# Kernel optimization log

Hardware: AMD Instinct MI355X
Metric: run time of the kernel (lower is better)

Reference implementation:

```python
import math
import jax, jax.numpy as jnp
import numpy as np

B, S, D = 64, 729, 64  # S = (32*14//16 - 1)**2

def setup_inputs() -> dict:
    key = jax.random.key(0)
    kq, kk, kv, km = jax.random.split(key, 4)
    return {
        "query": jax.random.normal(kq, (B, S, D), dtype=jnp.float32),
        "key": jax.random.normal(kk, (B, S, D), dtype=jnp.float32),
        "value": jax.random.normal(kv, (B, S, D), dtype=jnp.float32),
        "mask": jax.random.randint(km, (B, S, S), 0, 2, dtype=jnp.int32),
    }

def reference(query, key, value, mask):
    dk = query.shape[-1]
    # [B,S,S] scores
    scores = jnp.einsum('bqd,bkd->bqk', query, key) / math.sqrt(dk)
    scores = jnp.where(mask == 0, jnp.float32(-1e9), scores)
    attention = jnp.tanh(scores)  # args.activation == 'tanh'
    # ignore_diag == 1: zero the diagonal of each [S,S] attention map
    eye = jnp.eye(attention.shape[-1], dtype=attention.dtype)
    attention = attention * (1.0 - eye)
    out = jnp.einsum('bqk,bkd->bqd', attention, value)
    return (out, attention)
```

## Files before the change

### kernel.cpp

```cpp
#include <hip/hip_runtime.h>

#define BATCH 64
#define SEQ 729
#define DIM 64
#define NT 12
#define STRB 72
#define STRW 68

typedef __attribute__((ext_vector_type(8))) short bf16x8;
typedef __attribute__((ext_vector_type(4))) float f32x4;
typedef int   i32x4a __attribute__((ext_vector_type(4), aligned(4)));
typedef float f32x4a __attribute__((ext_vector_type(4), aligned(4)));

__device__ __forceinline__ unsigned short f2bf(float f) {
    unsigned int u = __float_as_uint(f);
    u += 0x7fffu + ((u >> 16) & 1u);
    return (unsigned short)(u >> 16);
}

__device__ __forceinline__ unsigned long long pack4bf(float a, float b, float c, float d) {
    return (unsigned long long)f2bf(a)
         | ((unsigned long long)f2bf(b) << 16)
         | ((unsigned long long)f2bf(c) << 32)
         | ((unsigned long long)f2bf(d) << 48);
}

__device__ __forceinline__ float fast_tanh(float x) {
    float e = __builtin_amdgcn_exp2f(x * 2.88539008177792681f);
    return 1.0f - 2.0f * __builtin_amdgcn_rcpf(e + 1.0f);
}

#define BAR() do { \
    asm volatile("s_waitcnt lgkmcnt(0)" ::: "memory"); \
    __builtin_amdgcn_s_barrier(); \
    __builtin_amdgcn_sched_barrier(0); \
} while (0)

__global__ __launch_bounds__(256, 3) void attn_kernel(
    const float* __restrict__ Qg, const float* __restrict__ Kg,
    const float* __restrict__ Vg, const int* __restrict__ Mg,
    float* __restrict__ Og, float* __restrict__ Ag)
{
    __shared__ unsigned short Ks[64 * STRB];
    __shared__ unsigned short Vs[64 * STRB];
    __shared__ unsigned short Qs[64 * STRB];
    __shared__ float Pf[64 * STRW];
    int* Mint = (int*)Pf;

    const int tid = threadIdx.x;
    const int q0  = blockIdx.x * 64;
    const int b   = blockIdx.y;

    const float* Qb = Qg + (size_t)b * SEQ * DIM;
    const float* Kb = Kg + (size_t)b * SEQ * DIM;
    const float* Vb = Vg + (size_t)b * SEQ * DIM;
    const int*   Mb = Mg + (size_t)b * SEQ * SEQ;
    float* Ob = Og + (size_t)b * SEQ * DIM;
    float* Ab = Ag + (size_t)b * SEQ * SEQ;

    const int lane = tid & 63;
    const int quad = lane >> 4;
    const int l15  = lane & 15;
    const int qrow = (tid >> 6) * 16;

    const int rr = tid >> 4;
    const int cc = (tid & 15) * 4;
    const int vd0 = (tid & 15) * 4;
    const int vk0 = (tid >> 4) * 4;
    const int prow = qrow + (lane >> 4);
    const int pcol = (lane & 15) * 4;

    float4 kr[4], vr[4];
    i32x4a mr[4];

    auto load_k = [&](int k0n) {
        #pragma unroll
        for (int i = 0; i < 4; ++i) {
            int gk = k0n + rr + 16 * i;
            kr[i] = (gk < SEQ) ? *(const float4*)(Kb + gk * DIM + cc)
                               : float4{0, 0, 0, 0};
        }
    };
    auto load_v = [&](int k0n) {
        #pragma unroll
        for (int i = 0; i < 4; ++i) {
            int gk = k0n + vk0 + i;
            vr[i] = (gk < SEQ) ? *(const float4*)(Vb + gk * DIM + vd0)
                               : float4{0, 0, 0, 0};
        }
    };
    auto load_mask = [&](int k0n) {
        #pragma unroll
        for (int i = 0; i < 4; ++i) {
            int gq = q0 + prow + 4 * i;
            int gk = k0n + pcol;
            if (gq < SEQ && gk + 3 < SEQ) {
                mr[i] = *(const i32x4a*)(Mb + (size_t)gq * SEQ + gk);
            } else if (gq < SEQ) {
                i32x4a t;
                #pragma unroll
                for (int e = 0; e < 4; ++e)
                    t[e] = (gk + e < SEQ) ? Mb[(size_t)gq * SEQ + gk + e] : 0;
                mr[i] = t;
            } else {
                mr[i] = i32x4a{0, 0, 0, 0};
            }
        }
    };
    auto drain_mask = [&]() {
        #pragma unroll
        for (int i = 0; i < 4; ++i)
            *(i32x4a*)&Mint[(prow + 4 * i) * STRW + pcol] = mr[i];
    };
    auto drain_kv = [&]() {
        #pragma unroll
        for (int i = 0; i < 4; ++i)
            *(unsigned long long*)&Ks[(rr + 16 * i) * STRB + cc] =
                pack4bf(kr[i].x, kr[i].y, kr[i].z, kr[i].w);
        #pragma unroll
        for (int j = 0; j < 4; ++j) {
            float v0 = j==0?vr[0].x:j==1?vr[0].y:j==2?vr[0].z:vr[0].w;
            float v1 = j==0?vr[1].x:j==1?vr[1].y:j==2?vr[1].z:vr[1].w;
            float v2 = j==0?vr[2].x:j==1?vr[2].y:j==2?vr[2].z:vr[2].w;
            float v3 = j==0?vr[3].x:j==1?vr[3].y:j==2?vr[3].z:vr[3].w;
            *(unsigned long long*)&Vs[(vd0 + j) * STRB + vk0] = pack4bf(v0, v1, v2, v3);
        }
    };

    #pragma unroll
    for (int i = 0; i < 4; ++i) {
        int gq = q0 + rr + 16 * i;
        float4 x = (gq < SEQ) ? *(const float4*)(Qb + gq * DIM + cc)
                              : float4{0, 0, 0, 0};
        *(unsigned long long*)&Qs[(rr + 16 * i) * STRB + cc] = pack4bf(x.x, x.y, x.z, x.w);
    }
    BAR();

    const bf16x8 aq0 = *(const bf16x8*)&Qs[(qrow + l15) * STRB + quad * 8];
    const bf16x8 aq1 = *(const bf16x8*)&Qs[(qrow + l15) * STRB + 32 + quad * 8];

    load_k(0); load_v(0); load_mask(0);

    f32x4 oacc[4];
    #pragma unroll
    for (int dt = 0; dt < 4; ++dt) {
        oacc[dt][0]=0.f; oacc[dt][1]=0.f; oacc[dt][2]=0.f; oacc[dt][3]=0.f;
    }

    for (int kt = 0; kt < NT; ++kt) {
        const int k0 = kt * 64;

        BAR();
        drain_mask();
        drain_kv();
        BAR();

        if (kt + 1 < NT) {
            load_k(k0 + 64); load_v(k0 + 64); load_mask(k0 + 64);
        }

        f32x4 sacc[4];
        #pragma unroll
        for (int nt2 = 0; nt2 < 4; ++nt2) {
            bf16x8 bk0 = *(const bf16x8*)&Ks[(nt2 * 16 + l15) * STRB + quad * 8];
            bf16x8 bk1 = *(const bf16x8*)&Ks[(nt2 * 16 + l15) * STRB + 32 + quad * 8];
            f32x4 c; c[0]=0.f; c[1]=0.f; c[2]=0.f; c[3]=0.f;
            c = __builtin_amdgcn_mfma_f32_16x16x32_bf16(aq0, bk0, c, 0, 0, 0);
            c = __builtin_amdgcn_mfma_f32_16x16x32_bf16(aq1, bk1, c, 0, 0, 0);
            sacc[nt2] = c;
        }

        #pragma unroll
        for (int nt2 = 0; nt2 < 4; ++nt2) {
            int col = nt2 * 16 + l15;
            int gk  = k0 + col;
            #pragma unroll
            for (int r = 0; r < 4; ++r) {
                int qloc = qrow + quad * 4 + r;
                int gq = q0 + qloc;
                int m = Mint[qloc * STRW + col];
                float sv = sacc[nt2][r] * 0.125f;
                bool msk = (m == 0);
                float p = fast_tanh(msk ? -1e9f : sv);
                if (msk) p = -1.0f;
                if (gq == gk) p = 0.0f;
                if (gq >= SEQ || gk >= SEQ) p = 0.0f;
                Pf[qloc * STRW + col] = p;
                Qs[qloc * STRB + col] = f2bf(p);
            }
        }

        #pragma unroll
        for (int i = 0; i < 4; ++i) {
            int row = prow + 4 * i;
            int gq  = q0 + row;
            int gk  = k0 + pcol;
            f32x4 pv = *(const f32x4*)&Pf[row * STRW + pcol];
            if (gq < SEQ) {
                if (gk + 3 < SEQ) {
                    *(f32x4a*)(Ab + (size_t)gq * SEQ + gk) = pv;
                } else {
                    #pragma unroll
                    for (int e = 0; e < 4; ++e)
                        if (gk + e < SEQ) Ab[(size_t)gq * SEQ + gk + e] = pv[e];
                }
            }
        }

        const bf16x8 ap0 = *(const bf16x8*)&Qs[(qrow + l15) * STRB + quad * 8];
        const bf16x8 ap1 = *(const bf16x8*)&Qs[(qrow + l15) * STRB + 32 + quad * 8];
        #pragma unroll
        for (int dt = 0; dt < 4; ++dt) {
            bf16x8 bv0 = *(const bf16x8*)&Vs[(dt * 16 + l15) * STRB + quad * 8];
            bf16x8 bv1 = *(const bf16x8*)&Vs[(dt * 16 + l15) * STRB + 32 + quad * 8];
            oacc[dt] = __builtin_amdgcn_mfma_f32_16x16x32_bf16(ap0, bv0, oacc[dt], 0, 0, 0);
            oacc[dt] = __builtin_amdgcn_mfma_f32_16x16x32_bf16(ap1, bv1, oacc[dt], 0, 0, 0);
        }
    }

    #pragma unroll
    for (int dt = 0; dt < 4; ++dt)
        #pragma unroll
        for (int r = 0; r < 4; ++r)
            Pf[(qrow + quad * 4 + r) * STRW + dt * 16 + l15] = oacc[dt][r];
    #pragma unroll
    for (int i = 0; i < 4; ++i) {
        int row = prow + 4 * i;
        int gq  = q0 + row;
        f32x4 ov = *(const f32x4*)&Pf[row * STRW + pcol];
        if (gq < SEQ) *(f32x4*)(Ob + (size_t)gq * DIM + pcol) = ov;
    }
}

extern "C" void kernel_launch(void* const* d_in, const int* in_sizes, int n_in,
                              void* d_out, int out_size, void* d_ws, size_t ws_size,
                              hipStream_t stream) {
    const float* Q = (const float*)d_in[0];
    const float* K = (const float*)d_in[1];
    const float* V = (const float*)d_in[2];
    const int*   M = (const int*)d_in[3];
    float* Out  = (float*)d_out;
    float* Attn = Out + (size_t)BATCH * SEQ * DIM;
    dim3 grid(NT, BATCH);
    attn_kernel<<<grid, 256, 0, stream>>>(Q, K, V, M, Out, Attn);
}
```

Baseline: 326.6 us.

## Preload mask as per-thread bitmasks and flush attention from bf16 staging

```diff
diff --git a/kernel.cpp b/kernel.cpp
--- a/kernel.cpp
+++ b/kernel.cpp
@@ -5,7 +5,9 @@
 #define DIM 64
 #define NT 12
 #define STRB 72
-#define STRW 68
+#define STRP 136
+#define MCH 772
+#define OSTR 68
 
 typedef __attribute__((ext_vector_type(8))) short bf16x8;
 typedef __attribute__((ext_vector_type(4))) float f32x4;
@@ -25,6 +27,10 @@
          | ((unsigned long long)f2bf(d) << 48);
 }
 
+__device__ __forceinline__ float bf2f(unsigned int hi16) {
+    return __uint_as_float(hi16 << 16);
+}
+
 __device__ __forceinline__ float fast_tanh(float x) {
     float e = __builtin_amdgcn_exp2f(x * 2.88539008177792681f);
     return 1.0f - 2.0f * __builtin_amdgcn_rcpf(e + 1.0f);
@@ -41,11 +47,12 @@
     const float* __restrict__ Vg, const int* __restrict__ Mg,
     float* __restrict__ Og, float* __restrict__ Ag)
 {
-    __shared__ unsigned short Ks[64 * STRB];
-    __shared__ unsigned short Vs[64 * STRB];
-    __shared__ unsigned short Qs[64 * STRB];
-    __shared__ float Pf[64 * STRW];
-    int* Mint = (int*)Pf;
+    __shared__ __align__(16) unsigned char smem[35840];
+    unsigned short* Ks = (unsigned short*)smem;
+    unsigned short* Vs = (unsigned short*)(smem + 9216);
+    unsigned short* Ps = (unsigned short*)(smem + 18432);
+    unsigned char*  Mc = smem;
+    float* Ostage = (float*)smem;
 
     const int tid = threadIdx.x;
     const int q0  = blockIdx.x * 64;
@@ -61,7 +68,8 @@
     const int lane = tid & 63;
     const int quad = lane >> 4;
     const int l15  = lane & 15;
-    const int qrow = (tid >> 6) * 16;
+    const int wid  = tid >> 6;
+    const int qrow = wid * 16;
 
     const int rr = tid >> 4;
     const int cc = (tid & 15) * 4;
@@ -71,7 +79,6 @@
     const int pcol = (lane & 15) * 4;
 
     float4 kr[4], vr[4];
-    i32x4a mr[4];
 
     auto load_k = [&](int k0n) {
         #pragma unroll
@@ -88,29 +95,6 @@
             vr[i] = (gk < SEQ) ? *(const float4*)(Vb + gk * DIM + vd0)
                                : float4{0, 0, 0, 0};
         }
-    };
-    auto load_mask = [&](int k0n) {
-        #pragma unroll
-        for (int i = 0; i < 4; ++i) {
-            int gq = q0 + prow + 4 * i;
-            int gk = k0n + pcol;
-            if (gq < SEQ && gk + 3 < SEQ) {
-                mr[i] = *(const i32x4a*)(Mb + (size_t)gq * SEQ + gk);
-            } else if (gq < SEQ) {
-                i32x4a t;
-                #pragma unroll
-                for (int e = 0; e < 4; ++e)
-                    t[e] = (gk + e < SEQ) ? Mb[(size_t)gq * SEQ + gk + e] : 0;
-                mr[i] = t;
-            } else {
-                mr[i] = i32x4a{0, 0, 0, 0};
-            }
-        }
-    };
-    auto drain_mask = [&]() {
-        #pragma unroll
-        for (int i = 0; i < 4; ++i)
-            *(i32x4a*)&Mint[(prow + 4 * i) * STRW + pcol] = mr[i];
     };
     auto drain_kv = [&]() {
         #pragma unroll
@@ -132,14 +116,49 @@
         int gq = q0 + rr + 16 * i;
         float4 x = (gq < SEQ) ? *(const float4*)(Qb + gq * DIM + cc)
                               : float4{0, 0, 0, 0};
-        *(unsigned long long*)&Qs[(rr + 16 * i) * STRB + cc] = pack4bf(x.x, x.y, x.z, x.w);
-    }
-    BAR();
-
-    const bf16x8 aq0 = *(const bf16x8*)&Qs[(qrow + l15) * STRB + quad * 8];
-    const bf16x8 aq1 = *(const bf16x8*)&Qs[(qrow + l15) * STRB + 32 + quad * 8];
-
-    load_k(0); load_v(0); load_mask(0);
+        *(unsigned long long*)&Ps[(rr + 16 * i) * STRP + cc] = pack4bf(x.x, x.y, x.z, x.w);
+    }
+
+    load_k(0); load_v(0);
+
+    unsigned mb[6] = {0, 0, 0, 0, 0, 0};
+    const int mg = tid >> 4;
+    const int ml = tid & 15;
+    for (int c = 0; c < 4; ++c) {
+        int grow = q0 + c * 16 + mg;
+        #pragma unroll
+        for (int it = 0; it < 12; ++it) {
+            int col = it * 64 + ml * 4;
+            i32x4a v = {0, 0, 0, 0};
+            if (grow < SEQ) {
+                if (col + 3 < SEQ) {
+                    v = *(const i32x4a*)(Mb + (size_t)grow * SEQ + col);
+                } else {
+                    #pragma unroll
+                    for (int e = 0; e < 4; ++e)
+                        if (col + e < SEQ) v[e] = Mb[(size_t)grow * SEQ + col + e];
+                }
+            }
+            unsigned by = (unsigned)(v[0] & 1) | ((unsigned)(v[1] & 1) << 8)
+                        | ((unsigned)(v[2] & 1) << 16) | ((unsigned)(v[3] & 1) << 24);
+            *(unsigned*)&Mc[mg * MCH + col] = by;
+        }
+        BAR();
+        if (wid == c) {
+            #pragma unroll
+            for (int t = 0; t < 12; ++t)
+                #pragma unroll
+                for (int n = 0; n < 4; ++n)
+                    #pragma unroll
+                    for (int r = 0; r < 4; ++r)
+                        if (Mc[(quad * 4 + r) * MCH + t * 64 + n * 16 + l15])
+                            mb[t >> 1] |= 1u << ((t & 1) * 16 + n * 4 + r);
+        }
+        BAR();
+    }
+
+    const bf16x8 aq0 = *(const bf16x8*)&Ps[(qrow + l15) * STRP + quad * 8];
+    const bf16x8 aq1 = *(const bf16x8*)&Ps[(qrow + l15) * STRP + 32 + quad * 8];
 
     f32x4 oacc[4];
     #pragma unroll
@@ -147,68 +166,46 @@
         oacc[dt][0]=0.f; oacc[dt][1]=0.f; oacc[dt][2]=0.f; oacc[dt][3]=0.f;
     }
 
-    for (int kt = 0; kt < NT; ++kt) {
-        const int k0 = kt * 64;
-
-        BAR();
-        drain_mask();
+    auto phase = [&](int t, unsigned half16, int toff) {
+        const int k0 = t * 64;
+
+        BAR();
         drain_kv();
         BAR();
 
-        if (kt + 1 < NT) {
-            load_k(k0 + 64); load_v(k0 + 64); load_mask(k0 + 64);
-        }
+        if (t + 1 < NT) { load_k(k0 + 64); load_v(k0 + 64); }
 
         f32x4 sacc[4];
         #pragma unroll
-        for (int nt2 = 0; nt2 < 4; ++nt2) {
-            bf16x8 bk0 = *(const bf16x8*)&Ks[(nt2 * 16 + l15) * STRB + quad * 8];
-            bf16x8 bk1 = *(const bf16x8*)&Ks[(nt2 * 16 + l15) * STRB + 32 + quad * 8];
-            f32x4 c; c[0]=0.f; c[1]=0.f; c[2]=0.f; c[3]=0.f;
-            c = __builtin_amdgcn_mfma_f32_16x16x32_bf16(aq0, bk0, c, 0, 0, 0);
-            c = __builtin_amdgcn_mfma_f32_16x16x32_bf16(aq1, bk1, c, 0, 0, 0);
-            sacc[nt2] = c;
-        }
-
-        #pragma unroll
-        for (int nt2 = 0; nt2 < 4; ++nt2) {
-            int col = nt2 * 16 + l15;
+        for (int n = 0; n < 4; ++n) {
+            bf16x8 bk0 = *(const bf16x8*)&Ks[(n * 16 + l15) * STRB + quad * 8];
+            bf16x8 bk1 = *(const bf16x8*)&Ks[(n * 16 + l15) * STRB + 32 + quad * 8];
+            f32x4 cacc; cacc[0]=0.f; cacc[1]=0.f; cacc[2]=0.f; cacc[3]=0.f;
+            cacc = __builtin_amdgcn_mfma_f32_16x16x32_bf16(aq0, bk0, cacc, 0, 0, 0);
+            cacc = __builtin_amdgcn_mfma_f32_16x16x32_bf16(aq1, bk1, cacc, 0, 0, 0);
+            sacc[n] = cacc;
+        }
+
+        #pragma unroll
+        for (int n = 0; n < 4; ++n) {
+            int col = n * 16 + l15;
             int gk  = k0 + col;
             #pragma unroll
             for (int r = 0; r < 4; ++r) {
                 int qloc = qrow + quad * 4 + r;
                 int gq = q0 + qloc;
-                int m = Mint[qloc * STRW + col];
-                float sv = sacc[nt2][r] * 0.125f;
-                bool msk = (m == 0);
+                bool msk = ((half16 >> (n * 4 + r)) & 1u) == 0u;
+                float sv = sacc[n][r] * 0.125f;
                 float p = fast_tanh(msk ? -1e9f : sv);
                 if (msk) p = -1.0f;
                 if (gq == gk) p = 0.0f;
                 if (gq >= SEQ || gk >= SEQ) p = 0.0f;
-                Pf[qloc * STRW + col] = p;
-                Qs[qloc * STRB + col] = f2bf(p);
+                Ps[qloc * STRP + toff + col] = f2bf(p);
             }
         }
 
-        #pragma unroll
-        for (int i = 0; i < 4; ++i) {
-            int row = prow + 4 * i;
-            int gq  = q0 + row;
-            int gk  = k0 + pcol;
-            f32x4 pv = *(const f32x4*)&Pf[row * STRW + pcol];
-            if (gq < SEQ) {
-                if (gk + 3 < SEQ) {
-                    *(f32x4a*)(Ab + (size_t)gq * SEQ + gk) = pv;
-                } else {
-                    #pragma unroll
-                    for (int e = 0; e < 4; ++e)
-                        if (gk + e < SEQ) Ab[(size_t)gq * SEQ + gk + e] = pv[e];
-                }
-            }
-        }
-
-        const bf16x8 ap0 = *(const bf16x8*)&Qs[(qrow + l15) * STRB + quad * 8];
-        const bf16x8 ap1 = *(const bf16x8*)&Qs[(qrow + l15) * STRB + 32 + quad * 8];
+        const bf16x8 ap0 = *(const bf16x8*)&Ps[(qrow + l15) * STRP + toff + quad * 8];
+        const bf16x8 ap1 = *(const bf16x8*)&Ps[(qrow + l15) * STRP + toff + 32 + quad * 8];
         #pragma unroll
         for (int dt = 0; dt < 4; ++dt) {
             bf16x8 bv0 = *(const bf16x8*)&Vs[(dt * 16 + l15) * STRB + quad * 8];
@@ -216,18 +213,54 @@
             oacc[dt] = __builtin_amdgcn_mfma_f32_16x16x32_bf16(ap0, bv0, oacc[dt], 0, 0, 0);
             oacc[dt] = __builtin_amdgcn_mfma_f32_16x16x32_bf16(ap1, bv1, oacc[dt], 0, 0, 0);
         }
-    }
-
+    };
+
+    auto flush = [&](int kt2) {
+        const int kbase = kt2 * 128;
+        #pragma unroll
+        for (int i = 0; i < 4; ++i) {
+            int row = prow + 4 * i;
+            int gq  = q0 + row;
+            if (gq >= SEQ) continue;
+            int gk = kbase + l15 * 8;
+            bf16x8 w = *(const bf16x8*)&Ps[row * STRP + l15 * 8];
+            float f0 = bf2f((unsigned short)w[0]), f1 = bf2f((unsigned short)w[1]);
+            float f2 = bf2f((unsigned short)w[2]), f3 = bf2f((unsigned short)w[3]);
+            float f4 = bf2f((unsigned short)w[4]), f5 = bf2f((unsigned short)w[5]);
+            float f6 = bf2f((unsigned short)w[6]), f7 = bf2f((unsigned short)w[7]);
+            if (gk + 7 < SEQ) {
+                f32x4a v0; v0[0]=f0; v0[1]=f1; v0[2]=f2; v0[3]=f3;
+                f32x4a v1; v1[0]=f4; v1[1]=f5; v1[2]=f6; v1[3]=f7;
+                *(f32x4a*)(Ab + (size_t)gq * SEQ + gk)     = v0;
+                *(f32x4a*)(Ab + (size_t)gq * SEQ + gk + 4) = v1;
+            } else {
+                float fe[8] = {f0,f1,f2,f3,f4,f5,f6,f7};
+                #pragma unroll
+                for (int e = 0; e < 8; ++e)
+                    if (gk + e < SEQ) Ab[(size_t)gq * SEQ + gk + e] = fe[e];
+            }
+        }
+    };
+
+    unsigned mw0 = mb[0], mw1 = mb[1], mw2 = mb[2], mw3 = mb[3], mw4 = mb[4], mw5 = mb[5];
+    for (int kt2 = 0; kt2 < 6; ++kt2) {
+        phase(2 * kt2,     mw0 & 0xffffu, 0);
+        phase(2 * kt2 + 1, mw0 >> 16,     64);
+        flush(kt2);
+        mw0 = mw1; mw1 = mw2; mw2 = mw3; mw3 = mw4; mw4 = mw5;
+    }
+
+    BAR();
     #pragma unroll
     for (int dt = 0; dt < 4; ++dt)
         #pragma unroll
         for (int r = 0; r < 4; ++r)
-            Pf[(qrow + quad * 4 + r) * STRW + dt * 16 + l15] = oacc[dt][r];
+            Ostage[(qrow + quad * 4 + r) * OSTR + dt * 16 + l15] = oacc[dt][r];
     #pragma unroll
     for (int i = 0; i < 4; ++i) {
         int row = prow + 4 * i;
         int gq  = q0 + row;
-        f32x4 ov = *(const f32x4*)&Pf[row * STRW + pcol];
+        f32x4 ov = *(const f32x4*)&Ostage[row * OSTR + pcol];
         if (gq < SEQ) *(f32x4*)(Ob + (size_t)gq * DIM + pcol) = ov;
     }
 }
```

Measured after the change: 332.2 us. About the same (+1.7%).
